# Performance work log

Hardware: AMD Instinct MI355X
Metric: run time of the kernel (lower is better)

Reference implementation:

```python
import jax, jax.numpy as jnp
import numpy as np

N_NODES = 50000
D_MODEL = 128
N_EDGES = 600000
HIDDEN = 128
EDGE_FEAT = 2 * D_MODEL + 2  # 258


def setup_inputs() -> dict:
    key = jax.random.key(0)
    k = jax.random.split(key, 8)
    H = jax.random.normal(k[0], (N_NODES, D_MODEL), dtype=jnp.float32)
    edge_index = jax.random.randint(k[1], (2, N_EDGES), 0, N_NODES, dtype=jnp.int64)
    S_e = jax.random.uniform(k[2], (N_EDGES,), dtype=jnp.float32)
    F_e = jax.random.uniform(k[3], (N_EDGES,), dtype=jnp.float32)
    W1 = jax.random.normal(k[4], (EDGE_FEAT, HIDDEN), dtype=jnp.float32) * (1.0 / np.sqrt(EDGE_FEAT))
    b1 = jnp.zeros((HIDDEN,), dtype=jnp.float32)
    W2 = jax.random.normal(k[5], (HIDDEN, 1), dtype=jnp.float32) * (1.0 / np.sqrt(HIDDEN))
    b2 = jnp.zeros((1,), dtype=jnp.float32)
    return {"H": H, "edge_index": edge_index, "S_e": S_e, "F_e": F_e,
            "W1": W1, "b1": b1, "W2": W2, "b2": b2}


def reference(H, edge_index, S_e, F_e, W1, b1, W2, b2):
    # Gather endpoint node features: [E, D]
    H_u = H[edge_index[0]]
    H_v = H[edge_index[1]]
    H_diff = jnp.abs(H_u - H_v)
    H_prod = H_u * H_v
    # [E, 2D+2]
    edge_features = jnp.concatenate(
        [H_diff, H_prod, S_e[:, None], F_e[:, None]], axis=1)
    # 2-layer MLP with SiLU (dropout is identity in eval mode)
    h = jax.nn.silu(edge_features @ W1 + b1)
    a_e = (h @ W2 + b2)[:, 0]  # [E]
    return a_e
```

## Files before the change

kernel.cpp:

```cpp
#include <hip/hip_runtime.h>


typedef _Float16       half8   __attribute__((ext_vector_type(8)));
typedef _Float16       half4v  __attribute__((ext_vector_type(4)));
typedef unsigned short ushort8 __attribute__((ext_vector_type(8)));
typedef float          f32x4   __attribute__((ext_vector_type(4)));

#define NSEG       8
#define W1T_STRIDE 288

__device__ __forceinline__ float silu_f(float x) {
    return x / (1.0f + __expf(-x));
}

__device__ __forceinline__ void canon(int u, int v, int& a, int& b) {
    const int sw = (u ^ v) & 1;
    a = sw ? v : u;
    b = sw ? u : v;
}


__global__ __launch_bounds__(256)
void cvt_hist_kernel(const float* __restrict__ H, _Float16* __restrict__ Hh,
                     int n4, const int* __restrict__ eidx,
                     int* __restrict__ hist, int E, int ASZ, int BBINS) {
    int i = blockIdx.x * blockDim.x + threadIdx.x;
    if (i < n4) {
        const float4 f = ((const float4*)H)[i];
        half4v h;
        h[0] = (_Float16)f.x; h[1] = (_Float16)f.y;
        h[2] = (_Float16)f.z; h[3] = (_Float16)f.w;
        ((half4v*)Hh)[i] = h;
    }
    if (i < E) {
        int a, b;
        canon(eidx[i], eidx[E + i], a, b);
        atomicAdd(&hist[(a / ASZ) * BBINS + (b >> 3)], 1);
    }
}

__global__ __launch_bounds__(256)
void scan1_kernel(int* __restrict__ hist, int* __restrict__ bsum, int NB) {
    __shared__ int s[256];
    const int t = threadIdx.x;
    const int i = blockIdx.x * 256 + t;
    const int v = (i < NB) ? hist[i] : 0;
    s[t] = v;
    __syncthreads();
    for (int off = 1; off < 256; off <<= 1) {
        const int x = (t >= off) ? s[t - off] : 0;
        __syncthreads();
        s[t] += x;
        __syncthreads();
    }
    if (i < NB) hist[i] = s[t] - v;
    if (t == 255) bsum[blockIdx.x] = s[255];
}

__global__ __launch_bounds__(256)
void scan2_kernel(int* __restrict__ bsum, int nb1,
                  const int* __restrict__ hist, int* __restrict__ vbs,
                  int BBINS, int E) {
    __shared__ int s[256];
    const int t = threadIdx.x;
    const int v = (t < nb1) ? bsum[t] : 0;
    s[t] = v;
    __syncthreads();
    for (int off = 1; off < 256; off <<= 1) {
        const int x = (t >= off) ? s[t - off] : 0;
        __syncthreads();
        s[t] += x;
        __syncthreads();
    }
    if (t < nb1) bsum[t] = s[t] - v;
    __syncthreads();
    if (t < NSEG) {
        const int idx = t * BBINS;
        vbs[t] = hist[idx] + bsum[idx >> 8];
    } else if (t == NSEG) {
        vbs[NSEG] = E;
    }
}

__global__ __launch_bounds__(256)
void scatter_kernel(const int* __restrict__ eidx, const float* __restrict__ Se,
                    const float* __restrict__ Fe, int* __restrict__ ofs,
                    const int* __restrict__ bsum,
                    int4* __restrict__ recs, int E, int ASZ, int BBINS) {
    int e = blockIdx.x * blockDim.x + threadIdx.x;
    if (e < E) {
        int a, b;
        canon(eidx[e], eidx[E + e], a, b);
        const int key = (a / ASZ) * BBINS + (b >> 3);
        const int pos = atomicAdd(&ofs[key], 1) + bsum[key >> 8];
        _Float16 sh = (_Float16)Se[e];
        _Float16 fh = (_Float16)Fe[e];
        unsigned pk = (unsigned)*(unsigned short*)&sh
                    | ((unsigned)*(unsigned short*)&fh << 16);
        recs[pos] = make_int4(a, b, e, (int)pk);
    }
}


__device__ __forceinline__ void stage_w1(const float* __restrict__ W1,
                                         const float* __restrict__ b1,
                                         _Float16* __restrict__ w1t, int tid) {
    const int n = tid & 127;
    const int g = tid >> 7;
    #pragma unroll
    for (int i = 0; i < 9; ++i) {
        const int kb = g + (i << 2);
        half8 tmp;
        if (kb < 32) {
            #pragma unroll
            for (int j = 0; j < 8; ++j) {
                const int kp  = (kb << 3) + j;
                const int c   = kp >> 5;
                const int k32 = kp & 31;
                const int src = ((c & 1) << 7) + ((c >> 1) << 5) + k32;
                tmp[j] = (_Float16)W1[src * 128 + n];
            }
            *(half8*)&w1t[n * W1T_STRIDE + ((kb ^ (n & 7)) << 3)] = tmp;
        } else {
            const int k32b = (kb - 32) << 3;
            #pragma unroll
            for (int j = 0; j < 8; ++j) {
                const int k32 = k32b + j;
                float v = 0.f;
                if (k32 == 0)      v = W1[32768 + n];
                else if (k32 == 1) v = W1[32896 + n];
                else if (k32 == 2) v = b1[n];
                tmp[j] = (_Float16)v;
            }
            *(half8*)&w1t[n * W1T_STRIDE + (kb << 3)] = tmp;
        }
    }
}


__device__ __forceinline__ void edge_tile16(
    const _Float16* __restrict__ Hh, const int4* __restrict__ recs,
    const _Float16* __restrict__ w1t,
    f32x4 w2a, f32x4 w2b, float b2v, float* __restrict__ out,
    int ebase, int elim, int q, int cb, int swz)
{
    const int e = min(ebase + cb, elim - 1);
    const int4 r = recs[e];
    const int a = r.x, b = r.y, oe = r.z;
    const unsigned pk = (unsigned)r.w;
    const unsigned short sl = (unsigned short)(pk & 0xFFFF);
    const unsigned short fl = (unsigned short)(pk >> 16);

    const _Float16* up = Hh + (size_t)a * 128;
    const _Float16* vp = Hh + (size_t)b * 128;

    f32x4 acc[8];
    #pragma unroll
    for (int t = 0; t < 8; ++t) acc[t] = (f32x4){0.f, 0.f, 0.f, 0.f};

    #pragma unroll
    for (int c8 = 0; c8 < 4; ++c8) {
        const half8 u8 = *(const half8*)(up + (c8 << 5) + (q << 3));
        const half8 v8 = *(const half8*)(vp + (c8 << 5) + (q << 3));
        half8 d8 = u8 - v8;
        ushort8 du = *(ushort8*)&d8;
        du = du & (unsigned short)0x7FFF;
        const half8 ae = *(half8*)&du;
        const half8 ao = u8 * v8;

        const int kb0 = ((c8 << 3) + q) ^ swz;
        const int kb1 = ((c8 << 3) + 4 + q) ^ swz;
        #pragma unroll
        for (int t = 0; t < 8; ++t) {
            const half8 b0 = *(const half8*)&w1t[((t << 4) + cb) * W1T_STRIDE + (kb0 << 3)];
            acc[t] = __builtin_amdgcn_mfma_f32_16x16x32_f16(ae, b0, acc[t], 0, 0, 0);
        }
        #pragma unroll
        for (int t = 0; t < 8; ++t) {
            const half8 b1f = *(const half8*)&w1t[((t << 4) + cb) * W1T_STRIDE + (kb1 << 3)];
            acc[t] = __builtin_amdgcn_mfma_f32_16x16x32_f16(ao, b1f, acc[t], 0, 0, 0);
        }
    }

    half8 aE;
    #pragma unroll
    for (int j = 0; j < 8; ++j) aE[j] = (_Float16)0.f;
    if (q == 0) {
        aE[0] = *(const _Float16*)&sl;
        aE[1] = *(const _Float16*)&fl;
        aE[2] = (_Float16)1.0f;
    }
    #pragma unroll
    for (int t = 0; t < 8; ++t) {
        const half8 bE = *(const half8*)&w1t[((t << 4) + cb) * W1T_STRIDE + ((32 + q) << 3)];
        acc[t] = __builtin_amdgcn_mfma_f32_16x16x32_f16(aE, bE, acc[t], 0, 0, 0);
    }

    int oe_r[4];
    #pragma unroll
    for (int rr = 0; rr < 4; ++rr) oe_r[rr] = __shfl(oe, (q << 2) + rr);

    float rs[4] = {0.f, 0.f, 0.f, 0.f};
    #pragma unroll
    for (int t = 0; t < 8; ++t) {
        const float w2c = (t < 4) ? w2a[t] : w2b[t - 4];
        const f32x4 av = acc[t];
        #pragma unroll
        for (int rr = 0; rr < 4; ++rr)
            rs[rr] += silu_f(av[rr]) * w2c;
    }

    #pragma unroll
    for (int off = 1; off < 16; off <<= 1) {
        #pragma unroll
        for (int rr = 0; rr < 4; ++rr) rs[rr] += __shfl_xor(rs[rr], off);
    }

    if (cb == 0) {
        #pragma unroll
        for (int rr = 0; rr < 4; ++rr) {
            const int pe = ebase + (q << 2) + rr;
            if (pe < elim) out[oe_r[rr]] = rs[rr] + b2v;
        }
    }
}


__global__ __launch_bounds__(512, 4)
void edgegate_seg(const _Float16* __restrict__ Hh,
                  const int4*  __restrict__ recs,
                  const int*   __restrict__ vbs,
                  int*         __restrict__ ctr,
                  const float* __restrict__ W1,
                  const float* __restrict__ b1,
                  const float* __restrict__ W2,
                  const float* __restrict__ b2,
                  float*       __restrict__ out)
{
    __shared__ _Float16 w1t[128 * W1T_STRIDE];
    __shared__ int tkt[2];
    const int tid = threadIdx.x;
    stage_w1(W1, b1, w1t, tid);

    int xcd;
    asm volatile("s_getreg_b32 %0, hwreg(HW_REG_XCC_ID)" : "=s"(xcd));
    xcd &= (NSEG - 1);

    const int lane = tid & 63;
    const int wave = tid >> 6;
    const int q    = lane >> 4;
    const int cb   = lane & 15;
    const int swz  = cb & 7;
    const float b2v = b2[0];
    f32x4 w2a, w2b;
    #pragma unroll
    for (int t = 0; t < 4; ++t) {
        w2a[t] = W2[(t << 4) + cb];
        w2b[t] = W2[((t + 4) << 4) + cb];
    }

    int p = 0;
    for (int sidx = 0; sidx < NSEG; ++sidx) {
        const int seg = (xcd + sidx) & (NSEG - 1);
        const int vs  = vbs[seg];
        const int ve  = vbs[seg + 1];
        const int ner = ve - vs;
        if (ner <= 0) continue;
        const int Tt = (ner + 127) >> 7;

        __syncthreads();
        if (tid == 0) tkt[p] = atomicAdd(&ctr[seg], 1);
        __syncthreads();
        int t0 = tkt[p];
        while (t0 < Tt) {
            const int pn = p ^ 1;
            if (tid == 0) tkt[pn] = atomicAdd(&ctr[seg], 1);
            const int ebase = vs + (t0 << 7) + (wave << 4);
            edge_tile16(Hh, recs, w1t, w2a, w2b, b2v, out, ebase, ve, q, cb, swz);
            __syncthreads();
            p = pn;
            t0 = tkt[p];
        }
    }
}


__global__ __launch_bounds__(512, 4)
void edgegate_fb(const float* __restrict__ H,
                 const _Float16* __restrict__ Hh,
                 const int*   __restrict__ eidx,
                 const float* __restrict__ Se,
                 const float* __restrict__ Fe,
                 const float* __restrict__ W1,
                 const float* __restrict__ b1,
                 const float* __restrict__ W2,
                 const float* __restrict__ b2,
                 float*       __restrict__ out,
                 int E, int ntiles, int useF16)
{
    __shared__ _Float16 w1t[128 * W1T_STRIDE];
    const int tid = threadIdx.x;
    stage_w1(W1, b1, w1t, tid);

    const int lane = tid & 63;
    const int wave = tid >> 6;
    const int q    = lane >> 4;
    const int cb   = lane & 15;
    const int swz  = cb & 7;
    const float b2v = b2[0];
    f32x4 w2a, w2b;
    #pragma unroll
    for (int t = 0; t < 4; ++t) {
        w2a[t] = W2[(t << 4) + cb];
        w2b[t] = W2[((t + 4) << 4) + cb];
    }

    __syncthreads();

    for (int tile = blockIdx.x; tile < ntiles; tile += gridDim.x) {
        const int ebase = tile * 128 + wave * 16;
        int e = ebase + cb;
        if (e >= E) e = E - 1;
        const int u = eidx[e];
        const int v = eidx[E + e];
        const float sfe = Se[e];
        const float ffe = Fe[e];

        f32x4 acc[8];
        #pragma unroll
        for (int t = 0; t < 8; ++t) acc[t] = (f32x4){0.f, 0.f, 0.f, 0.f};

        #pragma unroll
        for (int c8 = 0; c8 < 4; ++c8) {
            half8 ae, ao;
            if (useF16) {
                const _Float16* up = Hh + (size_t)u * 128;
                const _Float16* vp = Hh + (size_t)v * 128;
                const half8 u8 = *(const half8*)(up + (c8 << 5) + (q << 3));
                const half8 v8 = *(const half8*)(vp + (c8 << 5) + (q << 3));
                half8 d8 = u8 - v8;
                ushort8 du = *(ushort8*)&d8;
                du = du & (unsigned short)0x7FFF;
                ae = *(half8*)&du;
                ao = u8 * v8;
            } else {
                const float* up = H + (size_t)u * 128;
                const float* vp = H + (size_t)v * 128;
                #pragma unroll
                for (int j = 0; j < 8; ++j) {
                    const float uu = up[(c8 << 5) + (q << 3) + j];
                    const float vv = vp[(c8 << 5) + (q << 3) + j];
                    ae[j] = (_Float16)fabsf(uu - vv);
                    ao[j] = (_Float16)(uu * vv);
                }
            }
            const int kb0 = ((c8 << 3) + q) ^ swz;
            const int kb1 = ((c8 << 3) + 4 + q) ^ swz;
            #pragma unroll
            for (int t = 0; t < 8; ++t) {
                const half8 b0 = *(const half8*)&w1t[((t << 4) + cb) * W1T_STRIDE + (kb0 << 3)];
                acc[t] = __builtin_amdgcn_mfma_f32_16x16x32_f16(ae, b0, acc[t], 0, 0, 0);
            }
            #pragma unroll
            for (int t = 0; t < 8; ++t) {
                const half8 b1f = *(const half8*)&w1t[((t << 4) + cb) * W1T_STRIDE + (kb1 << 3)];
                acc[t] = __builtin_amdgcn_mfma_f32_16x16x32_f16(ao, b1f, acc[t], 0, 0, 0);
            }
        }

        half8 aE;
        #pragma unroll
        for (int j = 0; j < 8; ++j) aE[j] = (_Float16)0.f;
        if (q == 0) {
            aE[0] = (_Float16)sfe;
            aE[1] = (_Float16)ffe;
            aE[2] = (_Float16)1.0f;
        }
        #pragma unroll
        for (int t = 0; t < 8; ++t) {
            const half8 bE = *(const half8*)&w1t[((t << 4) + cb) * W1T_STRIDE + ((32 + q) << 3)];
            acc[t] = __builtin_amdgcn_mfma_f32_16x16x32_f16(aE, bE, acc[t], 0, 0, 0);
        }

        float rs[4] = {0.f, 0.f, 0.f, 0.f};
        #pragma unroll
        for (int t = 0; t < 8; ++t) {
            const float w2c = (t < 4) ? w2a[t] : w2b[t - 4];
            const f32x4 av = acc[t];
            #pragma unroll
            for (int rr = 0; rr < 4; ++rr)
                rs[rr] += silu_f(av[rr]) * w2c;
        }
        #pragma unroll
        for (int off = 1; off < 16; off <<= 1) {
            #pragma unroll
            for (int rr = 0; rr < 4; ++rr) rs[rr] += __shfl_xor(rs[rr], off);
        }

        const int e0 = ebase + (q << 2);
        if (cb == 0) {
            #pragma unroll
            for (int rr = 0; rr < 4; ++rr) {
                const int pe = e0 + rr;
                if (pe < E) out[pe] = rs[rr] + b2v;
            }
        }
    }
}


static inline size_t align256(size_t x) { return (x + 255) & ~(size_t)255; }

extern "C" void kernel_launch(void* const* d_in, const int* in_sizes, int n_in,
                              void* d_out, int out_size, void* d_ws, size_t ws_size,
                              hipStream_t stream)
{
    const float* H    = (const float*)d_in[0];
    const int*   eidx = (const int*)  d_in[1];
    const float* Se   = (const float*)d_in[2];
    const float* Fe   = (const float*)d_in[3];
    const float* W1   = (const float*)d_in[4];
    const float* b1   = (const float*)d_in[5];
    const float* W2   = (const float*)d_in[6];
    const float* b2   = (const float*)d_in[7];
    float* out = (float*)d_out;

    const int nH     = in_sizes[0];
    const int nNodes = nH / 128;
    const int E      = in_sizes[2];
    const int n4     = nH / 4;
    const int ntiles = (E + 127) / 128;

    const int ASZ   = (nNodes + NSEG - 1) / NSEG;
    const int BBINS = (nNodes + 7) >> 3;
    const int NB    = NSEG * BBINS;
    const int nb1   = (NB + 255) / 256;

    const size_t hhB    = (size_t)nH * sizeof(_Float16);
    const size_t off_g  = align256(hhB);
    const size_t off_bs = align256(off_g + (size_t)(NB + 8) * 4);
    const size_t off_vb = align256(off_bs + 256 * 4);
    const size_t off_r  = align256(off_vb + 16 * 4);
    const size_t need   = off_r + (size_t)E * sizeof(int4);

    if (ws_size >= need && nb1 <= 256) {
        _Float16* Hh   = (_Float16*)((char*)d_ws);
        int*      hist = (int*)     ((char*)d_ws + off_g);
        int*      ctr  = hist + NB;
        int*      bsum = (int*)     ((char*)d_ws + off_bs);
        int*      vbs  = (int*)     ((char*)d_ws + off_vb);
        int4*     recs = (int4*)    ((char*)d_ws + off_r);

        const int ncvh = (n4 > E) ? n4 : E;
        hipMemsetAsync(hist, 0, (size_t)(NB + 8) * sizeof(int), stream);
        hipLaunchKernelGGL(cvt_hist_kernel, dim3((ncvh + 255) / 256), dim3(256),
                           0, stream, H, Hh, n4, eidx, hist, E, ASZ, BBINS);
        hipLaunchKernelGGL(scan1_kernel, dim3(nb1), dim3(256), 0, stream,
                           hist, bsum, NB);
        hipLaunchKernelGGL(scan2_kernel, dim3(1), dim3(256), 0, stream,
                           bsum, nb1, hist, vbs, BBINS, E);
        hipLaunchKernelGGL(scatter_kernel, dim3((E + 255) / 256), dim3(256),
                           0, stream, eidx, Se, Fe, hist, bsum, recs,
                           E, ASZ, BBINS);
        hipLaunchKernelGGL(edgegate_seg, dim3(512), dim3(512), 0, stream,
                           Hh, recs, vbs, ctr, W1, b1, W2, b2, out);
    } else if (ws_size >= hhB) {
        _Float16* Hh = (_Float16*)d_ws;
        const int grid = (512 < ntiles) ? 512 : ntiles;
        hipLaunchKernelGGL(cvt_hist_kernel, dim3((n4 + 255) / 256), dim3(256),
                           0, stream, H, Hh, n4, eidx, (int*)nullptr, 0, 1, 1);
        hipLaunchKernelGGL(edgegate_fb, dim3(grid), dim3(512), 0, stream,
                           H, Hh, eidx, Se, Fe, W1, b1, W2, b2, out, E, ntiles, 1);
    } else {
        const int grid = (512 < ntiles) ? 512 : ntiles;
        hipLaunchKernelGGL(edgegate_fb, dim3(grid), dim3(512), 0, stream,
                           H, (const _Float16*)nullptr, eidx, Se, Fe, W1, b1, W2, b2,
                           out, E, ntiles, 0);
    }
}
```

Before: 282.9 us.

## Software-pipeline two edge tiles per wave and merge preprocessing kernels

The main gating kernel now claims 256-edge tickets and handles two 16-edge tiles per wave. The second tile's H gathers are issued before the first tile's epilogue, so gather latency overlaps the SiLU/reduction work, and the chunk order is rotated per wave. The two scan kernels become one using a last-block-done atomic pattern, and the fp16 conversion of H moves from the histogram pass into the scatter pass, removing one launch. The cost is higher register pressure from holding a second tile's operands, which may reduce occupancy.

New measurement: 770.9 us. 173% more time.

```diff
diff --git a/kernel.cpp b/kernel.cpp
--- a/kernel.cpp
+++ b/kernel.cpp
@@ -21,9 +21,64 @@
 
 
 __global__ __launch_bounds__(256)
-void cvt_hist_kernel(const float* __restrict__ H, _Float16* __restrict__ Hh,
-                     int n4, const int* __restrict__ eidx,
-                     int* __restrict__ hist, int E, int ASZ, int BBINS) {
+void hist_kernel(const int* __restrict__ eidx, int* __restrict__ hist,
+                 int E, int ASZ, int BBINS) {
+    int e = blockIdx.x * blockDim.x + threadIdx.x;
+    if (e < E) {
+        int a, b;
+        canon(eidx[e], eidx[E + e], a, b);
+        atomicAdd(&hist[(a / ASZ) * BBINS + (b >> 3)], 1);
+    }
+}
+
+__global__ __launch_bounds__(256)
+void scan_kernel(int* __restrict__ hist, int* __restrict__ bsum,
+                 int NB, int nb1, int* __restrict__ flag,
+                 int* __restrict__ vbs, int BBINS, int E) {
+    __shared__ int s[256];
+    __shared__ int lastBlk;
+    const int t = threadIdx.x;
+    const int i = blockIdx.x * 256 + t;
+    const int v = (i < NB) ? hist[i] : 0;
+    s[t] = v;
+    __syncthreads();
+    for (int off = 1; off < 256; off <<= 1) {
+        const int x = (t >= off) ? s[t - off] : 0;
+        __syncthreads();
+        s[t] += x;
+        __syncthreads();
+    }
+    if (i < NB) hist[i] = s[t] - v;
+    if (t == 255) bsum[blockIdx.x] = s[255];
+    __threadfence();
+    if (t == 0) lastBlk = (atomicAdd(flag, 1) == (int)gridDim.x - 1);
+    __syncthreads();
+    if (!lastBlk) return;
+    const int bv = (t < nb1) ? atomicAdd(&bsum[t], 0) : 0;
+    s[t] = bv;
+    __syncthreads();
+    for (int off = 1; off < 256; off <<= 1) {
+        const int x = (t >= off) ? s[t - off] : 0;
+        __syncthreads();
+        s[t] += x;
+        __syncthreads();
+    }
+    if (t < nb1) bsum[t] = s[t] - bv;
+    __syncthreads();
+    if (t < NSEG) {
+        const int idx = t * BBINS;
+        vbs[t] = atomicAdd(&hist[idx], 0) + bsum[idx >> 8];
+    } else if (t == NSEG) {
+        vbs[NSEG] = E;
+    }
+}
+
+__global__ __launch_bounds__(256)
+void scatter_cvt_kernel(const float* __restrict__ H, _Float16* __restrict__ Hh,
+                        int n4, const int* __restrict__ eidx,
+                        const float* __restrict__ Se, const float* __restrict__ Fe,
+                        int* __restrict__ ofs, const int* __restrict__ bsum,
+                        int4* __restrict__ recs, int E, int ASZ, int BBINS) {
     int i = blockIdx.x * blockDim.x + threadIdx.x;
     if (i < n4) {
         const float4 f = ((const float4*)H)[i];
@@ -35,69 +90,13 @@
     if (i < E) {
         int a, b;
         canon(eidx[i], eidx[E + i], a, b);
-        atomicAdd(&hist[(a / ASZ) * BBINS + (b >> 3)], 1);
-    }
-}
-
-__global__ __launch_bounds__(256)
-void scan1_kernel(int* __restrict__ hist, int* __restrict__ bsum, int NB) {
-    __shared__ int s[256];
-    const int t = threadIdx.x;
-    const int i = blockIdx.x * 256 + t;
-    const int v = (i < NB) ? hist[i] : 0;
-    s[t] = v;
-    __syncthreads();
-    for (int off = 1; off < 256; off <<= 1) {
-        const int x = (t >= off) ? s[t - off] : 0;
-        __syncthreads();
-        s[t] += x;
-        __syncthreads();
-    }
-    if (i < NB) hist[i] = s[t] - v;
-    if (t == 255) bsum[blockIdx.x] = s[255];
-}
-
-__global__ __launch_bounds__(256)
-void scan2_kernel(int* __restrict__ bsum, int nb1,
-                  const int* __restrict__ hist, int* __restrict__ vbs,
-                  int BBINS, int E) {
-    __shared__ int s[256];
-    const int t = threadIdx.x;
-    const int v = (t < nb1) ? bsum[t] : 0;
-    s[t] = v;
-    __syncthreads();
-    for (int off = 1; off < 256; off <<= 1) {
-        const int x = (t >= off) ? s[t - off] : 0;
-        __syncthreads();
-        s[t] += x;
-        __syncthreads();
-    }
-    if (t < nb1) bsum[t] = s[t] - v;
-    __syncthreads();
-    if (t < NSEG) {
-        const int idx = t * BBINS;
-        vbs[t] = hist[idx] + bsum[idx >> 8];
-    } else if (t == NSEG) {
-        vbs[NSEG] = E;
-    }
-}
-
-__global__ __launch_bounds__(256)
-void scatter_kernel(const int* __restrict__ eidx, const float* __restrict__ Se,
-                    const float* __restrict__ Fe, int* __restrict__ ofs,
-                    const int* __restrict__ bsum,
-                    int4* __restrict__ recs, int E, int ASZ, int BBINS) {
-    int e = blockIdx.x * blockDim.x + threadIdx.x;
-    if (e < E) {
-        int a, b;
-        canon(eidx[e], eidx[E + e], a, b);
         const int key = (a / ASZ) * BBINS + (b >> 3);
         const int pos = atomicAdd(&ofs[key], 1) + bsum[key >> 8];
-        _Float16 sh = (_Float16)Se[e];
-        _Float16 fh = (_Float16)Fe[e];
+        _Float16 sh = (_Float16)Se[i];
+        _Float16 fh = (_Float16)Fe[i];
         unsigned pk = (unsigned)*(unsigned short*)&sh
                     | ((unsigned)*(unsigned short*)&fh << 16);
-        recs[pos] = make_int4(a, b, e, (int)pk);
+        recs[pos] = make_int4(a, b, i, (int)pk);
     }
 }
 
@@ -138,30 +137,19 @@
 }
 
 
-__device__ __forceinline__ void edge_tile16(
-    const _Float16* __restrict__ Hh, const int4* __restrict__ recs,
-    const _Float16* __restrict__ w1t,
-    f32x4 w2a, f32x4 w2b, float b2v, float* __restrict__ out,
-    int ebase, int elim, int q, int cb, int swz)
+__device__ __forceinline__ void mfma_tile(
+    f32x4 acc[8], const half8* __restrict__ u, const half8* __restrict__ v,
+    unsigned pk, const _Float16* __restrict__ w1t,
+    int q, int cb, int swz, int wave)
 {
-    const int e = min(ebase + cb, elim - 1);
-    const int4 r = recs[e];
-    const int a = r.x, b = r.y, oe = r.z;
-    const unsigned pk = (unsigned)r.w;
-    const unsigned short sl = (unsigned short)(pk & 0xFFFF);
-    const unsigned short fl = (unsigned short)(pk >> 16);
-
-    const _Float16* up = Hh + (size_t)a * 128;
-    const _Float16* vp = Hh + (size_t)b * 128;
-
-    f32x4 acc[8];
     #pragma unroll
     for (int t = 0; t < 8; ++t) acc[t] = (f32x4){0.f, 0.f, 0.f, 0.f};
 
     #pragma unroll
-    for (int c8 = 0; c8 < 4; ++c8) {
-        const half8 u8 = *(const half8*)(up + (c8 << 5) + (q << 3));
-        const half8 v8 = *(const half8*)(vp + (c8 << 5) + (q << 3));
+    for (int i = 0; i < 4; ++i) {
+        const int c8 = (i + wave) & 3;
+        const half8 u8 = u[i];
+        const half8 v8 = v[i];
         half8 d8 = u8 - v8;
         ushort8 du = *(ushort8*)&d8;
         du = du & (unsigned short)0x7FFF;
@@ -182,6 +170,8 @@
         }
     }
 
+    const unsigned short sl = (unsigned short)(pk & 0xFFFF);
+    const unsigned short fl = (unsigned short)(pk >> 16);
     half8 aE;
     #pragma unroll
     for (int j = 0; j < 8; ++j) aE[j] = (_Float16)0.f;
@@ -195,7 +185,12 @@
         const half8 bE = *(const half8*)&w1t[((t << 4) + cb) * W1T_STRIDE + ((32 + q) << 3)];
         acc[t] = __builtin_amdgcn_mfma_f32_16x16x32_f16(aE, bE, acc[t], 0, 0, 0);
     }
-
+}
+
+__device__ __forceinline__ void epilogue_tile(
+    const f32x4 acc[8], int oe, f32x4 w2a, f32x4 w2b, float b2v,
+    float* __restrict__ out, int ebase, int elim, int q, int cb)
+{
     int oe_r[4];
     #pragma unroll
     for (int rr = 0; rr < 4; ++rr) oe_r[rr] = __shfl(oe, (q << 2) + rr);
@@ -209,13 +204,11 @@
         for (int rr = 0; rr < 4; ++rr)
             rs[rr] += silu_f(av[rr]) * w2c;
     }
-
     #pragma unroll
     for (int off = 1; off < 16; off <<= 1) {
         #pragma unroll
         for (int rr = 0; rr < 4; ++rr) rs[rr] += __shfl_xor(rs[rr], off);
     }
-
     if (cb == 0) {
         #pragma unroll
         for (int rr = 0; rr < 4; ++rr) {
@@ -266,7 +259,7 @@
         const int ve  = vbs[seg + 1];
         const int ner = ve - vs;
         if (ner <= 0) continue;
-        const int Tt = (ner + 127) >> 7;
+        const int Tt = (ner + 255) >> 8;
 
         __syncthreads();
         if (tid == 0) tkt[p] = atomicAdd(&ctr[seg], 1);
@@ -275,8 +268,39 @@
         while (t0 < Tt) {
             const int pn = p ^ 1;
             if (tid == 0) tkt[pn] = atomicAdd(&ctr[seg], 1);
-            const int ebase = vs + (t0 << 7) + (wave << 4);
-            edge_tile16(Hh, recs, w1t, w2a, w2b, b2v, out, ebase, ve, q, cb, swz);
+
+            const int eA = vs + (t0 << 8) + (wave << 4);
+            const int eB = eA + 128;
+            const int4 rA = recs[min(eA + cb, ve - 1)];
+            const int4 rB = recs[min(eB + cb, ve - 1)];
+
+            const _Float16* upA = Hh + (size_t)rA.x * 128;
+            const _Float16* vpA = Hh + (size_t)rA.y * 128;
+            half8 uA[4], vA[4];
+            #pragma unroll
+            for (int i = 0; i < 4; ++i) {
+                const int c8 = (i + wave) & 3;
+                uA[i] = *(const half8*)(upA + (c8 << 5) + (q << 3));
+                vA[i] = *(const half8*)(vpA + (c8 << 5) + (q << 3));
+            }
+            f32x4 accA[8];
+            mfma_tile(accA, uA, vA, (unsigned)rA.w, w1t, q, cb, swz, wave);
+
+            const _Float16* upB = Hh + (size_t)rB.x * 128;
+            const _Float16* vpB = Hh + (size_t)rB.y * 128;
+            half8 uB[4], vB[4];
+            #pragma unroll
+            for (int i = 0; i < 4; ++i) {
+                const int c8 = (i + wave) & 3;
+                uB[i] = *(const half8*)(upB + (c8 << 5) + (q << 3));
+                vB[i] = *(const half8*)(vpB + (c8 << 5) + (q << 3));
+            }
+            epilogue_tile(accA, rA.z, w2a, w2b, b2v, out, eA, ve, q, cb);
+
+            f32x4 accB[8];
+            mfma_tile(accB, uB, vB, (unsigned)rB.w, w1t, q, cb, swz, wave);
+            epilogue_tile(accB, rB.z, w2a, w2b, b2v, out, eB, ve, q, cb);
+
             __syncthreads();
             p = pn;
             t0 = tkt[p];
@@ -323,88 +347,39 @@
         if (e >= E) e = E - 1;
         const int u = eidx[e];
         const int v = eidx[E + e];
-        const float sfe = Se[e];
-        const float ffe = Fe[e];
-
-        f32x4 acc[8];
-        #pragma unroll
-        for (int t = 0; t < 8; ++t) acc[t] = (f32x4){0.f, 0.f, 0.f, 0.f};
-
-        #pragma unroll
-        for (int c8 = 0; c8 < 4; ++c8) {
-            half8 ae, ao;
-            if (useF16) {
-                const _Float16* up = Hh + (size_t)u * 128;
-                const _Float16* vp = Hh + (size_t)v * 128;
-                const half8 u8 = *(const half8*)(up + (c8 << 5) + (q << 3));
-                const half8 v8 = *(const half8*)(vp + (c8 << 5) + (q << 3));
-                half8 d8 = u8 - v8;
-                ushort8 du = *(ushort8*)&d8;
-                du = du & (unsigned short)0x7FFF;
-                ae = *(half8*)&du;
-                ao = u8 * v8;
-            } else {
-                const float* up = H + (size_t)u * 128;
-                const float* vp = H + (size_t)v * 128;
+        _Float16 sh = (_Float16)Se[e];
+        _Float16 fh = (_Float16)Fe[e];
+        unsigned pk = (unsigned)*(unsigned short*)&sh
+                    | ((unsigned)*(unsigned short*)&fh << 16);
+
+        half8 u4[4], v4[4];
+        if (useF16) {
+            const _Float16* up = Hh + (size_t)u * 128;
+            const _Float16* vp = Hh + (size_t)v * 128;
+            #pragma unroll
+            for (int i = 0; i < 4; ++i) {
+                const int c8 = (i + wave) & 3;
+                u4[i] = *(const half8*)(up + (c8 << 5) + (q << 3));
+                v4[i] = *(const half8*)(vp + (c8 << 5) + (q << 3));
+            }
+        } else {
+            const float* up = H + (size_t)u * 128;
+            const float* vp = H + (size_t)v * 128;
+            #pragma unroll
+            for (int i = 0; i < 4; ++i) {
+                const int c8 = (i + wave) & 3;
                 #pragma unroll
                 for (int j = 0; j < 8; ++j) {
-                    const float uu = up[(c8 << 5) + (q << 3) + j];
-                    const float vv = vp[(c8 << 5) + (q << 3) + j];
-                    ae[j] = (_Float16)fabsf(uu - vv);
-                    ao[j] = (_Float16)(uu * vv);
+                    u4[i][j] = (_Float16)up[(c8 << 5) + (q << 3) + j];
+                    v4[i][j] = (_Float16)vp[(c8 << 5) + (q << 3) + j];
                 }
             }
-            const int kb0 = ((c8 << 3) + q) ^ swz;
-            const int kb1 = ((c8 << 3) + 4 + q) ^ swz;
-            #pragma unroll
-            for (int t = 0; t < 8; ++t) {
-                const half8 b0 = *(const half8*)&w1t[((t << 4) + cb) * W1T_STRIDE + (kb0 << 3)];
-                acc[t] = __builtin_amdgcn_mfma_f32_16x16x32_f16(ae, b0, acc[t], 0, 0, 0);
-            }
-            #pragma unroll
-            for (int t = 0; t < 8; ++t) {
-                const half8 b1f = *(const half8*)&w1t[((t << 4) + cb) * W1T_STRIDE + (kb1 << 3)];
-                acc[t] = __builtin_amdgcn_mfma_f32_16x16x32_f16(ao, b1f, acc[t], 0, 0, 0);
-            }
-        }
-
-        half8 aE;
-        #pragma unroll
-        for (int j = 0; j < 8; ++j) aE[j] = (_Float16)0.f;
-        if (q == 0) {
-            aE[0] = (_Float16)sfe;
-            aE[1] = (_Float16)ffe;
-            aE[2] = (_Float16)1.0f;
-        }
-        #pragma unroll
-        for (int t = 0; t < 8; ++t) {
-            const half8 bE = *(const half8*)&w1t[((t << 4) + cb) * W1T_STRIDE + ((32 + q) << 3)];
-            acc[t] = __builtin_amdgcn_mfma_f32_16x16x32_f16(aE, bE, acc[t], 0, 0, 0);
-        }
-
-        float rs[4] = {0.f, 0.f, 0.f, 0.f};
-        #pragma unroll
-        for (int t = 0; t < 8; ++t) {
-            const float w2c = (t < 4) ? w2a[t] : w2b[t - 4];
-            const f32x4 av = acc[t];
-            #pragma unroll
-            for (int rr = 0; rr < 4; ++rr)
-                rs[rr] += silu_f(av[rr]) * w2c;
-        }
-        #pragma unroll
-        for (int off = 1; off < 16; off <<= 1) {
-            #pragma unroll
-            for (int rr = 0; rr < 4; ++rr) rs[rr] += __shfl_xor(rs[rr], off);
-        }
-
-        const int e0 = ebase + (q << 2);
-        if (cb == 0) {
-            #pragma unroll
-            for (int rr = 0; rr < 4; ++rr) {
-                const int pe = e0 + rr;
-                if (pe < E) out[pe] = rs[rr] + b2v;
-            }
-        }
+        }
+
+        f32x4 acc[8];
+        mfma_tile(acc, u4, v4, pk, w1t, q, cb, swz, wave);
+
+        epilogue_tile(acc, e, w2a, w2b, b2v, out, ebase, E, q, cb);
     }
 }
 
@@ -438,7 +413,7 @@
 
     const size_t hhB    = (size_t)nH * sizeof(_Float16);
     const size_t off_g  = align256(hhB);
-    const size_t off_bs = align256(off_g + (size_t)(NB + 8) * 4);
+    const size_t off_bs = align256(off_g + (size_t)(NB + 16) * 4);
     const size_t off_vb = align256(off_bs + 256 * 4);
     const size_t off_r  = align256(off_vb + 16 * 4);
     const size_t need   = off_r + (size_t)E * sizeof(int4);
@@ -447,28 +422,29 @@
         _Float16* Hh   = (_Float16*)((char*)d_ws);
         int*      hist = (int*)     ((char*)d_ws + off_g);
         int*      ctr  = hist + NB;
+        int*      flag = hist + NB + 8;
         int*      bsum = (int*)     ((char*)d_ws + off_bs);
         int*      vbs  = (int*)     ((char*)d_ws + off_vb);
         int4*     recs = (int4*)    ((char*)d_ws + off_r);
 
-        const int ncvh = (n4 > E) ? n4 : E;
-        hipMemsetAsync(hist, 0, (size_t)(NB + 8) * sizeof(int), stream);
-        hipLaunchKernelGGL(cvt_hist_kernel, dim3((ncvh + 255) / 256), dim3(256),
-                           0, stream, H, Hh, n4, eidx, hist, E, ASZ, BBINS);
-        hipLaunchKernelGGL(scan1_kernel, dim3(nb1), dim3(256), 0, stream,
-                           hist, bsum, NB);
-        hipLaunchKernelGGL(scan2_kernel, dim3(1), dim3(256), 0, stream,
-                           bsum, nb1, hist, vbs, BBINS, E);
-        hipLaunchKernelGGL(scatter_kernel, dim3((E + 255) / 256), dim3(256),
-                           0, stream, eidx, Se, Fe, hist, bsum, recs,
+        hipMemsetAsync(hist, 0, (size_t)(NB + 16) * sizeof(int), stream);
+        hipLaunchKernelGGL(hist_kernel, dim3((E + 255) / 256), dim3(256),
+                           0, stream, eidx, hist, E, ASZ, BBINS);
+        hipLaunchKernelGGL(scan_kernel, dim3(nb1), dim3(256), 0, stream,
+                           hist, bsum, NB, nb1, flag, vbs, BBINS, E);
+        hipLaunchKernelGGL(scatter_cvt_kernel, dim3((n4 + 255) / 256), dim3(256),
+                           0, stream, H, Hh, n4, eidx, Se, Fe, hist, bsum, recs,
                            E, ASZ, BBINS);
         hipLaunchKernelGGL(edgegate_seg, dim3(512), dim3(512), 0, stream,
                            Hh, recs, vbs, ctr, W1, b1, W2, b2, out);
     } else if (ws_size >= hhB) {
         _Float16* Hh = (_Float16*)d_ws;
         const int grid = (512 < ntiles) ? 512 : ntiles;
-        hipLaunchKernelGGL(cvt_hist_kernel, dim3((n4 + 255) / 256), dim3(256),
-                           0, stream, H, Hh, n4, eidx, (int*)nullptr, 0, 1, 1);
+        hipLaunchKernelGGL(scatter_cvt_kernel, dim3((n4 + 255) / 256), dim3(256),
+                           0, stream, H, Hh, n4, (const int*)nullptr,
+                           (const float*)nullptr, (const float*)nullptr,
+                           (int*)nullptr, (const int*)nullptr, (int4*)nullptr,
+                           0, 1, 1);
         hipLaunchKernelGGL(edgegate_fb, dim3(grid), dim3(512), 0, stream,
                            H, Hh, eidx, Se, Fe, W1, b1, W2, b2, out, E, ntiles, 1);
     } else {
```

## Fuse two-pass scan via last-block pattern, move H conversion into scatter, rotate chunk order

Applied to the files above, without the earlier changes.

The two scan kernels become one: the last block to finish, detected with an atomic counter, scans the block sums and writes the segment bounds. The H fp32→fp16 conversion moves from the histogram kernel into the scatter kernel, so the histogram kernel only walks edges. Both edge kernels now start their K-chunk loop at an offset that depends on the wave index, which spreads concurrent gather and LDS accesses across waves. This removes one kernel launch and some serialization, at the cost of a threadfence plus atomic handshake in the scan.

Result: slower. 296.0 us (+4.6%).

```diff
diff --git a/kernel.cpp b/kernel.cpp
--- a/kernel.cpp
+++ b/kernel.cpp
@@ -21,9 +21,64 @@
 
 
 __global__ __launch_bounds__(256)
-void cvt_hist_kernel(const float* __restrict__ H, _Float16* __restrict__ Hh,
-                     int n4, const int* __restrict__ eidx,
-                     int* __restrict__ hist, int E, int ASZ, int BBINS) {
+void hist_kernel(const int* __restrict__ eidx, int* __restrict__ hist,
+                 int E, int ASZ, int BBINS) {
+    int e = blockIdx.x * blockDim.x + threadIdx.x;
+    if (e < E) {
+        int a, b;
+        canon(eidx[e], eidx[E + e], a, b);
+        atomicAdd(&hist[(a / ASZ) * BBINS + (b >> 3)], 1);
+    }
+}
+
+__global__ __launch_bounds__(256)
+void scan_kernel(int* __restrict__ hist, int* __restrict__ bsum,
+                 int NB, int nb1, int* __restrict__ flag,
+                 int* __restrict__ vbs, int BBINS, int E) {
+    __shared__ int s[256];
+    __shared__ int lastBlk;
+    const int t = threadIdx.x;
+    const int i = blockIdx.x * 256 + t;
+    const int v = (i < NB) ? hist[i] : 0;
+    s[t] = v;
+    __syncthreads();
+    for (int off = 1; off < 256; off <<= 1) {
+        const int x = (t >= off) ? s[t - off] : 0;
+        __syncthreads();
+        s[t] += x;
+        __syncthreads();
+    }
+    if (i < NB) hist[i] = s[t] - v;
+    if (t == 255) bsum[blockIdx.x] = s[255];
+    __threadfence();
+    if (t == 0) lastBlk = (atomicAdd(flag, 1) == (int)gridDim.x - 1);
+    __syncthreads();
+    if (!lastBlk) return;
+    const int bv = (t < nb1) ? atomicAdd(&bsum[t], 0) : 0;
+    s[t] = bv;
+    __syncthreads();
+    for (int off = 1; off < 256; off <<= 1) {
+        const int x = (t >= off) ? s[t - off] : 0;
+        __syncthreads();
+        s[t] += x;
+        __syncthreads();
+    }
+    if (t < nb1) bsum[t] = s[t] - bv;
+    __syncthreads();
+    if (t < NSEG) {
+        const int idx = t * BBINS;
+        vbs[t] = atomicAdd(&hist[idx], 0) + bsum[idx >> 8];
+    } else if (t == NSEG) {
+        vbs[NSEG] = E;
+    }
+}
+
+__global__ __launch_bounds__(256)
+void scatter_cvt_kernel(const float* __restrict__ H, _Float16* __restrict__ Hh,
+                        int n4, const int* __restrict__ eidx,
+                        const float* __restrict__ Se, const float* __restrict__ Fe,
+                        int* __restrict__ ofs, const int* __restrict__ bsum,
+                        int4* __restrict__ recs, int E, int ASZ, int BBINS) {
     int i = blockIdx.x * blockDim.x + threadIdx.x;
     if (i < n4) {
         const float4 f = ((const float4*)H)[i];
@@ -35,69 +90,13 @@
     if (i < E) {
         int a, b;
         canon(eidx[i], eidx[E + i], a, b);
-        atomicAdd(&hist[(a / ASZ) * BBINS + (b >> 3)], 1);
-    }
-}
-
-__global__ __launch_bounds__(256)
-void scan1_kernel(int* __restrict__ hist, int* __restrict__ bsum, int NB) {
-    __shared__ int s[256];
-    const int t = threadIdx.x;
-    const int i = blockIdx.x * 256 + t;
-    const int v = (i < NB) ? hist[i] : 0;
-    s[t] = v;
-    __syncthreads();
-    for (int off = 1; off < 256; off <<= 1) {
-        const int x = (t >= off) ? s[t - off] : 0;
-        __syncthreads();
-        s[t] += x;
-        __syncthreads();
-    }
-    if (i < NB) hist[i] = s[t] - v;
-    if (t == 255) bsum[blockIdx.x] = s[255];
-}
-
-__global__ __launch_bounds__(256)
-void scan2_kernel(int* __restrict__ bsum, int nb1,
-                  const int* __restrict__ hist, int* __restrict__ vbs,
-                  int BBINS, int E) {
-    __shared__ int s[256];
-    const int t = threadIdx.x;
-    const int v = (t < nb1) ? bsum[t] : 0;
-    s[t] = v;
-    __syncthreads();
-    for (int off = 1; off < 256; off <<= 1) {
-        const int x = (t >= off) ? s[t - off] : 0;
-        __syncthreads();
-        s[t] += x;
-        __syncthreads();
-    }
-    if (t < nb1) bsum[t] = s[t] - v;
-    __syncthreads();
-    if (t < NSEG) {
-        const int idx = t * BBINS;
-        vbs[t] = hist[idx] + bsum[idx >> 8];
-    } else if (t == NSEG) {
-        vbs[NSEG] = E;
-    }
-}
-
-__global__ __launch_bounds__(256)
-void scatter_kernel(const int* __restrict__ eidx, const float* __restrict__ Se,
-                    const float* __restrict__ Fe, int* __restrict__ ofs,
-                    const int* __restrict__ bsum,
-                    int4* __restrict__ recs, int E, int ASZ, int BBINS) {
-    int e = blockIdx.x * blockDim.x + threadIdx.x;
-    if (e < E) {
-        int a, b;
-        canon(eidx[e], eidx[E + e], a, b);
         const int key = (a / ASZ) * BBINS + (b >> 3);
         const int pos = atomicAdd(&ofs[key], 1) + bsum[key >> 8];
-        _Float16 sh = (_Float16)Se[e];
-        _Float16 fh = (_Float16)Fe[e];
+        _Float16 sh = (_Float16)Se[i];
+        _Float16 fh = (_Float16)Fe[i];
         unsigned pk = (unsigned)*(unsigned short*)&sh
                     | ((unsigned)*(unsigned short*)&fh << 16);
-        recs[pos] = make_int4(a, b, e, (int)pk);
+        recs[pos] = make_int4(a, b, i, (int)pk);
     }
 }
 
@@ -142,7 +141,7 @@
     const _Float16* __restrict__ Hh, const int4* __restrict__ recs,
     const _Float16* __restrict__ w1t,
     f32x4 w2a, f32x4 w2b, float b2v, float* __restrict__ out,
-    int ebase, int elim, int q, int cb, int swz)
+    int ebase, int elim, int q, int cb, int swz, int wave)
 {
     const int e = min(ebase + cb, elim - 1);
     const int4 r = recs[e];
@@ -159,7 +158,8 @@
     for (int t = 0; t < 8; ++t) acc[t] = (f32x4){0.f, 0.f, 0.f, 0.f};
 
     #pragma unroll
-    for (int c8 = 0; c8 < 4; ++c8) {
+    for (int i = 0; i < 4; ++i) {
+        const int c8 = (i + wave) & 3;
         const half8 u8 = *(const half8*)(up + (c8 << 5) + (q << 3));
         const half8 v8 = *(const half8*)(vp + (c8 << 5) + (q << 3));
         half8 d8 = u8 - v8;
@@ -276,7 +276,8 @@
             const int pn = p ^ 1;
             if (tid == 0) tkt[pn] = atomicAdd(&ctr[seg], 1);
             const int ebase = vs + (t0 << 7) + (wave << 4);
-            edge_tile16(Hh, recs, w1t, w2a, w2b, b2v, out, ebase, ve, q, cb, swz);
+            edge_tile16(Hh, recs, w1t, w2a, w2b, b2v, out, ebase, ve,
+                        q, cb, swz, wave);
             __syncthreads();
             p = pn;
             t0 = tkt[p];
@@ -331,7 +332,8 @@
         for (int t = 0; t < 8; ++t) acc[t] = (f32x4){0.f, 0.f, 0.f, 0.f};
 
         #pragma unroll
-        for (int c8 = 0; c8 < 4; ++c8) {
+        for (int i = 0; i < 4; ++i) {
+            const int c8 = (i + wave) & 3;
             half8 ae, ao;
             if (useF16) {
                 const _Float16* up = Hh + (size_t)u * 128;
@@ -438,7 +440,7 @@
 
     const size_t hhB    = (size_t)nH * sizeof(_Float16);
     const size_t off_g  = align256(hhB);
-    const size_t off_bs = align256(off_g + (size_t)(NB + 8) * 4);
+    const size_t off_bs = align256(off_g + (size_t)(NB + 16) * 4);
     const size_t off_vb = align256(off_bs + 256 * 4);
     const size_t off_r  = align256(off_vb + 16 * 4);
     const size_t need   = off_r + (size_t)E * sizeof(int4);
@@ -447,28 +449,29 @@
         _Float16* Hh   = (_Float16*)((char*)d_ws);
         int*      hist = (int*)     ((char*)d_ws + off_g);
         int*      ctr  = hist + NB;
+        int*      flag = hist + NB + 8;
         int*      bsum = (int*)     ((char*)d_ws + off_bs);
         int*      vbs  = (int*)     ((char*)d_ws + off_vb);
         int4*     recs = (int4*)    ((char*)d_ws + off_r);
 
-        const int ncvh = (n4 > E) ? n4 : E;
-        hipMemsetAsync(hist, 0, (size_t)(NB + 8) * sizeof(int), stream);
-        hipLaunchKernelGGL(cvt_hist_kernel, dim3((ncvh + 255) / 256), dim3(256),
-                           0, stream, H, Hh, n4, eidx, hist, E, ASZ, BBINS);
-        hipLaunchKernelGGL(scan1_kernel, dim3(nb1), dim3(256), 0, stream,
-                           hist, bsum, NB);
-        hipLaunchKernelGGL(scan2_kernel, dim3(1), dim3(256), 0, stream,
-                           bsum, nb1, hist, vbs, BBINS, E);
-        hipLaunchKernelGGL(scatter_kernel, dim3((E + 255) / 256), dim3(256),
-                           0, stream, eidx, Se, Fe, hist, bsum, recs,
+        hipMemsetAsync(hist, 0, (size_t)(NB + 16) * sizeof(int), stream);
+        hipLaunchKernelGGL(hist_kernel, dim3((E + 255) / 256), dim3(256),
+                           0, stream, eidx, hist, E, ASZ, BBINS);
+        hipLaunchKernelGGL(scan_kernel, dim3(nb1), dim3(256), 0, stream,
+                           hist, bsum, NB, nb1, flag, vbs, BBINS, E);
+        hipLaunchKernelGGL(scatter_cvt_kernel, dim3((n4 + 255) / 256), dim3(256),
+                           0, stream, H, Hh, n4, eidx, Se, Fe, hist, bsum, recs,
                            E, ASZ, BBINS);
         hipLaunchKernelGGL(edgegate_seg, dim3(512), dim3(512), 0, stream,
                            Hh, recs, vbs, ctr, W1, b1, W2, b2, out);
     } else if (ws_size >= hhB) {
         _Float16* Hh = (_Float16*)d_ws;
         const int grid = (512 < ntiles) ? 512 : ntiles;
-        hipLaunchKernelGGL(cvt_hist_kernel, dim3((n4 + 255) / 256), dim3(256),
-                           0, stream, H, Hh, n4, eidx, (int*)nullptr, 0, 1, 1);
+        hipLaunchKernelGGL(scatter_cvt_kernel, dim3((n4 + 255) / 256), dim3(256),
+                           0, stream, H, Hh, n4, (const int*)nullptr,
+                           (const float*)nullptr, (const float*)nullptr,
+                           (int*)nullptr, (const int*)nullptr, (int4*)nullptr,
+                           0, 1, 1);
         hipLaunchKernelGGL(edgegate_fb, dim3(grid), dim3(512), 0, stream,
                            H, Hh, eidx, Se, Fe, W1, b1, W2, b2, out, E, ntiles, 1);
     } else {
```
